# Optimization experiments

Hardware: AMD Instinct MI355X
Metric: run time of the kernel (lower is better)

Reference implementation:

```python
import jax, jax.numpy as jnp
import numpy as np

D_MODEL = 1024
HEADS = 16
HEAD_DIM = D_MODEL // HEADS


def setup_inputs() -> dict:
    key = jax.random.key(0)
    k_x, k_q, k_k, k_v, k_o = jax.random.split(key, 5)
    B, S = 4, 2048
    return {
        "x": jax.random.normal(k_x, (B, S, D_MODEL), dtype=jnp.float32),
        "W_q": jax.random.normal(k_q, (D_MODEL, D_MODEL), dtype=jnp.float32),
        "W_k": jax.random.normal(k_k, (D_MODEL, D_MODEL), dtype=jnp.float32),
        "W_v": jax.random.normal(k_v, (D_MODEL, D_MODEL), dtype=jnp.float32),
        "fc_out": jax.random.normal(k_o, (D_MODEL, D_MODEL), dtype=jnp.float32),
    }


def reference(x, W_q, W_k, W_v, fc_out):
    B, S, D = x.shape
    H, Hd = HEADS, HEAD_DIM
    # QKV projections (no bias)
    Q = jnp.matmul(x, W_q)  # [B,S,D]
    K = jnp.matmul(x, W_k)
    V = jnp.matmul(x, W_v)
    # split heads -> [B,H,S,Hd]
    Qh = Q.reshape(B, S, H, Hd).transpose(0, 2, 1, 3)
    Kh = K.reshape(B, S, H, Hd).transpose(0, 2, 1, 3)
    Vh = V.reshape(B, S, H, Hd).transpose(0, 2, 1, 3)
    # full unfused attention: materialize [B,H,S,S] scores, softmax over last dim
    scores = jnp.einsum("bhqd,bhkd->bhqk", Qh, Kh) / jnp.sqrt(jnp.float32(Hd))
    attn = jax.nn.softmax(scores, axis=-1)
    head_out = jnp.einsum("bhqk,bhkd->bhqd", attn, Vh)  # [B,H,S,Hd]
    merged = head_out.transpose(0, 2, 1, 3).reshape(B, S, D)
    return jnp.matmul(merged, fc_out)
```

## Files before the change

### kernel.cpp

```cpp
#include <hip/hip_runtime.h>
#include <stdint.h>

#define MROWS 8192
#define DM    1024
#define NH    16
#define HD    64
#define SEQ   2048

typedef __bf16 bf16x8 __attribute__((ext_vector_type(8)));
typedef __bf16 bf16x4 __attribute__((ext_vector_type(4)));
typedef float  floatx4 __attribute__((ext_vector_type(4)));

#define QSCALE 0.18033688011112042f

__device__ __forceinline__ int xcd_swz512(int bid) {
  return ((bid & 7) << 6) | (bid >> 3);
}

__device__ __forceinline__ void async16(const void* g, void* l) {
  __builtin_amdgcn_global_load_lds(
      (__attribute__((address_space(1))) void*)g,
      (__attribute__((address_space(3))) void*)l,
      16, 0, 0);
}

__device__ __forceinline__ floatx4 mfma16(bf16x8 a, bf16x8 b, floatx4 c) {
  return __builtin_amdgcn_mfma_f32_16x16x32_bf16(a, b, c, 0, 0, 0);
}


__global__ void __launch_bounds__(256) split_x_kernel(const float* __restrict__ x,
                                                      __bf16* __restrict__ xh,
                                                      __bf16* __restrict__ xl) {
  const int i = blockIdx.x * 256 + threadIdx.x;
  const float4 v = reinterpret_cast<const float4*>(x)[i];
  const float vv[4] = {v.x, v.y, v.z, v.w};
  bf16x4 H, L;
#pragma unroll
  for (int j = 0; j < 4; ++j) {
    const __bf16 h = (__bf16)vv[j];
    H[j] = h;
    L[j] = (__bf16)(vv[j] - (float)h);
  }
  reinterpret_cast<bf16x4*>(xh)[i] = H;
  reinterpret_cast<bf16x4*>(xl)[i] = L;
}

__global__ void __launch_bounds__(256) wtrans4_kernel(
    const float* __restrict__ Wq, const float* __restrict__ Wk,
    const float* __restrict__ Wv, const float* __restrict__ Wf,
    __bf16* __restrict__ Tqh, __bf16* __restrict__ Tql,
    __bf16* __restrict__ Tkh, __bf16* __restrict__ Tkl,
    __bf16* __restrict__ Tvh, __bf16* __restrict__ Tfh) {
  const int which = blockIdx.x >> 10;
  const int blk = blockIdx.x & 1023;
  const float* W = (which == 0) ? Wq : (which == 1) ? Wk : (which == 2) ? Wv : Wf;
  __bf16* Th = (which == 0) ? Tqh : (which == 1) ? Tkh : (which == 2) ? Tvh : Tfh;
  __bf16* Tl = (which == 0) ? Tql : (which == 1) ? Tkl : (__bf16*)nullptr;

  __shared__ float t[32][33];
  const int tx = threadIdx.x & 31, ty = threadIdx.x >> 5;
  const int bx = blk & 31, by = blk >> 5;
#pragma unroll
  for (int j = 0; j < 4; ++j) {
    const int k = by * 32 + ty + j * 8;
    t[ty + j * 8][tx] = W[(size_t)k * DM + bx * 32 + tx];
  }
  __syncthreads();
#pragma unroll
  for (int j = 0; j < 4; ++j) {
    const int n = bx * 32 + ty + j * 8;
    const int k = by * 32 + tx;
    const float v = t[tx][ty + j * 8];
    const __bf16 h = (__bf16)v;
    Th[(size_t)n * DM + k] = h;
    if (Tl) Tl[(size_t)n * DM + k] = (__bf16)(v - (float)h);
  }
}

template <int OUTMODE>
__global__ void __launch_bounds__(256) gemm_nt(const __bf16* __restrict__ Ah,
                                               const __bf16* __restrict__ Bh,
                                               void* __restrict__ C0) {
  __shared__ __align__(16) __bf16 sAh[128 * 32];
  __shared__ __align__(16) __bf16 sBh[128 * 32];

  const int tid = threadIdx.x;
  const int lid = xcd_swz512(blockIdx.x);
  const int bm = lid >> 3;
  const int bn = lid & 7;
  const int m0 = bm << 7, n0 = bn << 7;
  const int w = tid >> 6;
  const int lane = tid & 63;
  const int wm = (w >> 1) << 6;
  const int wn = (w & 1) << 6;
  const int lm = lane & 15;
  const int q4 = lane >> 4;

  floatx4 acc[4][4];
  const floatx4 fz = {0.f, 0.f, 0.f, 0.f};
#pragma unroll
  for (int i = 0; i < 4; ++i)
#pragma unroll
    for (int j = 0; j < 4; ++j) acc[i][j] = fz;

  const int c0 = tid, c1 = tid + 256;
  const int row0 = c0 >> 2, cc0 = (c0 & 3) ^ ((row0 >> 1) & 3);
  const int row1 = c1 >> 2, cc1 = (c1 & 3) ^ ((row1 >> 1) & 3);

  int offA[4], offB[4];
#pragma unroll
  for (int i = 0; i < 4; ++i) {
    const int ra = wm + i * 16 + lm;
    offA[i] = ra * 32 + ((q4 ^ ((ra >> 1) & 3)) << 3);
    const int rb = wn + i * 16 + lm;
    offB[i] = rb * 32 + ((q4 ^ ((rb >> 1) & 3)) << 3);
  }

  size_t ga0 = (size_t)(m0 + row0) * DM + cc0 * 8;
  size_t gb0 = (size_t)(n0 + row0) * DM + cc0 * 8;
  size_t ga1 = (size_t)(m0 + row1) * DM + cc1 * 8;
  size_t gb1 = (size_t)(n0 + row1) * DM + cc1 * 8;

  for (int it = 0; it < 32; ++it) {
    async16(Ah + ga0, &sAh[c0 * 8]);
    async16(Bh + gb0, &sBh[c0 * 8]);
    async16(Ah + ga1, &sAh[c1 * 8]);
    async16(Bh + gb1, &sBh[c1 * 8]);
    ga0 += 32; gb0 += 32; ga1 += 32; gb1 += 32;
    __syncthreads();

    bf16x8 ah[4], bh[4];
#pragma unroll
    for (int i = 0; i < 4; ++i) {
      ah[i] = *(const bf16x8*)&sAh[offA[i]];
      bh[i] = *(const bf16x8*)&sBh[offB[i]];
    }
#pragma unroll
    for (int i = 0; i < 4; ++i)
#pragma unroll
      for (int j = 0; j < 4; ++j)
        acc[i][j] = mfma16(ah[i], bh[j], acc[i][j]);
    __syncthreads();
  }

#pragma unroll
  for (int i = 0; i < 4; ++i) {
#pragma unroll
    for (int j = 0; j < 4; ++j) {
#pragma unroll
      for (int r = 0; r < 4; ++r) {
        const int gr = m0 + wm + i * 16 + q4 * 4 + r;
        const int gc = n0 + wn + j * 16 + lm;
        const float v = acc[i][j][r];
        if constexpr (OUTMODE == 1) {
          ((float*)C0)[(size_t)gr * DM + gc] = v;
        } else {
          const int bb = gr >> 11, ss = gr & 2047;
          const int s6 = ss & 63;
          const int sp = (ss & ~63) | (s6 & 32) | ((s6 & 12) << 1) |
                         ((s6 & 16) >> 2) | (s6 & 3);
          const int hh = gc >> 6, dd = gc & 63;
          ((__bf16*)C0)[(((size_t)(bb * NH + hh) << 6) + dd) * SEQ + sp] = (__bf16)v;
        }
      }
    }
  }
}

__global__ void __launch_bounds__(256, 2) gemm_qk(const __bf16* __restrict__ Ah,
                                                  const __bf16* __restrict__ Al,
                                                  const __bf16* __restrict__ Bqh,
                                                  const __bf16* __restrict__ Bql,
                                                  const __bf16* __restrict__ Bkh,
                                                  const __bf16* __restrict__ Bkl,
                                                  __bf16* __restrict__ Qh,
                                                  __bf16* __restrict__ Ql,
                                                  __bf16* __restrict__ Kh,
                                                  __bf16* __restrict__ Kl) {
  __shared__ __align__(16) __bf16 sAh[128 * 32];
  __shared__ __align__(16) __bf16 sAl[128 * 32];
  __shared__ __align__(16) __bf16 sQh_[128 * 32];
  __shared__ __align__(16) __bf16 sQl_[128 * 32];
  __shared__ __align__(16) __bf16 sKh_[128 * 32];
  __shared__ __align__(16) __bf16 sKl_[128 * 32];

  const int tid = threadIdx.x;
  const int lid = xcd_swz512(blockIdx.x);
  const int bm = lid >> 3;
  const int bn = lid & 7;
  const int m0 = bm << 7, n0 = bn << 7;
  const int w = tid >> 6;
  const int lane = tid & 63;
  const int wm = (w >> 1) << 6;
  const int wn = (w & 1) << 6;
  const int lm = lane & 15;
  const int q4 = lane >> 4;

  floatx4 accq[4][4], acck[4][4];
  const floatx4 fz = {0.f, 0.f, 0.f, 0.f};
#pragma unroll
  for (int i = 0; i < 4; ++i)
#pragma unroll
    for (int j = 0; j < 4; ++j) { accq[i][j] = fz; acck[i][j] = fz; }

  const int c0 = tid, c1 = tid + 256;
  const int row0 = c0 >> 2, cc0 = (c0 & 3) ^ ((row0 >> 1) & 3);
  const int row1 = c1 >> 2, cc1 = (c1 & 3) ^ ((row1 >> 1) & 3);

  int offA[4], offB[4];
#pragma unroll
  for (int i = 0; i < 4; ++i) {
    const int ra = wm + i * 16 + lm;
    offA[i] = ra * 32 + ((q4 ^ ((ra >> 1) & 3)) << 3);
    const int rb = wn + i * 16 + lm;
    offB[i] = rb * 32 + ((q4 ^ ((rb >> 1) & 3)) << 3);
  }

  size_t ga0 = (size_t)(m0 + row0) * DM + cc0 * 8;
  size_t gb0 = (size_t)(n0 + row0) * DM + cc0 * 8;
  size_t ga1 = (size_t)(m0 + row1) * DM + cc1 * 8;
  size_t gb1 = (size_t)(n0 + row1) * DM + cc1 * 8;

  for (int it = 0; it < 32; ++it) {
    async16(Ah + ga0, &sAh[c0 * 8]);
    async16(Al + ga0, &sAl[c0 * 8]);
    async16(Ah + ga1, &sAh[c1 * 8]);
    async16(Al + ga1, &sAl[c1 * 8]);
    async16(Bqh + gb0, &sQh_[c0 * 8]);
    async16(Bql + gb0, &sQl_[c0 * 8]);
    async16(Bqh + gb1, &sQh_[c1 * 8]);
    async16(Bql + gb1, &sQl_[c1 * 8]);
    async16(Bkh + gb0, &sKh_[c0 * 8]);
    async16(Bkl + gb0, &sKl_[c0 * 8]);
    async16(Bkh + gb1, &sKh_[c1 * 8]);
    async16(Bkl + gb1, &sKl_[c1 * 8]);
    ga0 += 32; gb0 += 32; ga1 += 32; gb1 += 32;
    __syncthreads();

    bf16x8 ah[4], al[4];
#pragma unroll
    for (int i = 0; i < 4; ++i) {
      ah[i] = *(const bf16x8*)&sAh[offA[i]];
      al[i] = *(const bf16x8*)&sAl[offA[i]];
    }
    {
      bf16x8 bh[4], bl[4];
#pragma unroll
      for (int j = 0; j < 4; ++j) {
        bh[j] = *(const bf16x8*)&sQh_[offB[j]];
        bl[j] = *(const bf16x8*)&sQl_[offB[j]];
      }
#pragma unroll
      for (int i = 0; i < 4; ++i)
#pragma unroll
        for (int j = 0; j < 4; ++j) {
          accq[i][j] = mfma16(ah[i], bh[j], accq[i][j]);
          accq[i][j] = mfma16(ah[i], bl[j], accq[i][j]);
          accq[i][j] = mfma16(al[i], bh[j], accq[i][j]);
        }
    }
    {
      bf16x8 bh[4], bl[4];
#pragma unroll
      for (int j = 0; j < 4; ++j) {
        bh[j] = *(const bf16x8*)&sKh_[offB[j]];
        bl[j] = *(const bf16x8*)&sKl_[offB[j]];
      }
#pragma unroll
      for (int i = 0; i < 4; ++i)
#pragma unroll
        for (int j = 0; j < 4; ++j) {
          acck[i][j] = mfma16(ah[i], bh[j], acck[i][j]);
          acck[i][j] = mfma16(ah[i], bl[j], acck[i][j]);
          acck[i][j] = mfma16(al[i], bh[j], acck[i][j]);
        }
    }
    __syncthreads();
  }

#pragma unroll
  for (int i = 0; i < 4; ++i) {
#pragma unroll
    for (int j = 0; j < 4; ++j) {
#pragma unroll
      for (int r = 0; r < 4; ++r) {
        const int gr = m0 + wm + i * 16 + q4 * 4 + r;
        const int gc = n0 + wn + j * 16 + lm;
        const size_t idx = (size_t)gr * DM + gc;
        const float vq = accq[i][j][r] * QSCALE;
        const __bf16 qhv = (__bf16)vq;
        Qh[idx] = qhv;
        Ql[idx] = (__bf16)(vq - (float)qhv);
        const float vk = acck[i][j][r];
        const __bf16 khv = (__bf16)vk;
        Kh[idx] = khv;
        Kl[idx] = (__bf16)(vk - (float)khv);
      }
    }
  }
}

__global__ void __launch_bounds__(256, 2) flash_kernel(const __bf16* __restrict__ Qh,
                                                       const __bf16* __restrict__ Ql,
                                                       const __bf16* __restrict__ Kh,
                                                       const __bf16* __restrict__ Kl,
                                                       const __bf16* __restrict__ Vt,
                                                       __bf16* __restrict__ Mg) {
  __shared__ __align__(16) __bf16 sKh[2][64 * 64];
  __shared__ __align__(16) __bf16 sKl[2][64 * 64];
  __shared__ __align__(16) __bf16 sV[2][64 * 64];

  const int tid = threadIdx.x;
  const int lid = xcd_swz512(blockIdx.x);
  const int qt = lid & 7;
  const int bh = lid >> 3;
  const int b = bh >> 4;
  const int h = bh & 15;
  const int mq0 = b * SEQ + qt * 256;
  const int ch = h * 64;
  const int w = tid >> 6;
  const int lane = tid & 63;
  const int lm = lane & 15;
  const int q4 = lane >> 4;

  const int c0 = tid, c1 = tid + 256;
  const int r0 = c0 >> 3, e0 = ((c0 & 7) ^ (r0 & 7)) << 3;
  const int r1 = c1 >> 3, e1 = ((c1 & 7) ^ (r1 & 7)) << 3;

  bf16x8 qh[4][2], ql[4][2];
#pragma unroll
  for (int p = 0; p < 4; ++p) {
    const size_t gq0 = (size_t)(mq0 + p * 64 + r0) * DM + ch + e0;
    const size_t gq1 = (size_t)(mq0 + p * 64 + r1) * DM + ch + e1;
    async16(Qh + gq0, &sKh[0][c0 * 8]);
    async16(Ql + gq0, &sKl[0][c0 * 8]);
    async16(Qh + gq1, &sKh[0][c1 * 8]);
    async16(Ql + gq1, &sKl[0][c1 * 8]);
    __syncthreads();
    if (w == p) {
#pragma unroll
      for (int mi = 0; mi < 4; ++mi) {
        const int rq = mi * 16 + lm;
#pragma unroll
        for (int ks = 0; ks < 2; ++ks) {
          const int oq = rq * 64 + (((ks * 4 + q4) ^ (rq & 7)) << 3);
          qh[mi][ks] = *(const bf16x8*)&sKh[0][oq];
          ql[mi][ks] = *(const bf16x8*)&sKl[0][oq];
        }
      }
    }
    __syncthreads();
  }

  int ofr[2][4];
#pragma unroll
  for (int ks = 0; ks < 2; ++ks)
#pragma unroll
    for (int t = 0; t < 4; ++t) {
      const int rk = t * 16 + lm;
      ofr[ks][t] = rk * 64 + (((ks * 4 + q4) ^ (rk & 7)) << 3);
    }

  floatx4 o[4][4];
  const floatx4 fz = {0.f, 0.f, 0.f, 0.f};
#pragma unroll
  for (int mi = 0; mi < 4; ++mi)
#pragma unroll
    for (int dt = 0; dt < 4; ++dt) o[mi][dt] = fz;
  float lsum[4] = {0.f, 0.f, 0.f, 0.f};
  float m[4] = {-1e30f, -1e30f, -1e30f, -1e30f};

  size_t gk0 = (size_t)(b * SEQ + r0) * DM + ch + e0;
  size_t gk1 = (size_t)(b * SEQ + r1) * DM + ch + e1;
  size_t gv0 = (size_t)(bh * 64 + r0) * SEQ + e0;
  size_t gv1 = (size_t)(bh * 64 + r1) * SEQ + e1;

  async16(Kh + gk0, &sKh[0][c0 * 8]);
  async16(Kl + gk0, &sKl[0][c0 * 8]);
  async16(Kh + gk1, &sKh[0][c1 * 8]);
  async16(Kl + gk1, &sKl[0][c1 * 8]);
  async16(Vt + gv0, &sV[0][c0 * 8]);
  async16(Vt + gv1, &sV[0][c1 * 8]);
  gk0 += (size_t)64 * DM;
  gk1 += (size_t)64 * DM;
  gv0 += 64;
  gv1 += 64;

  for (int it = 0; it < 32; ++it) {
    const int cur = it & 1;
    asm volatile("s_waitcnt vmcnt(0)" ::: "memory");
    __builtin_amdgcn_s_barrier();
    __builtin_amdgcn_sched_barrier(0);
    if (it < 31) {
      const int nxt = cur ^ 1;
      async16(Kh + gk0, &sKh[nxt][c0 * 8]);
      async16(Kl + gk0, &sKl[nxt][c0 * 8]);
      async16(Kh + gk1, &sKh[nxt][c1 * 8]);
      async16(Kl + gk1, &sKl[nxt][c1 * 8]);
      async16(Vt + gv0, &sV[nxt][c0 * 8]);
      async16(Vt + gv1, &sV[nxt][c1 * 8]);
      gk0 += (size_t)64 * DM;
      gk1 += (size_t)64 * DM;
      gv0 += 64;
      gv1 += 64;
    }
    const __bf16* bKh = sKh[cur];
    const __bf16* bKl = sKl[cur];
    const __bf16* bV = sV[cur];

    floatx4 s2[4][4];
#pragma unroll
    for (int nt = 0; nt < 4; ++nt)
#pragma unroll
      for (int mi = 0; mi < 4; ++mi) s2[nt][mi] = fz;
#pragma unroll
    for (int ks = 0; ks < 2; ++ks) {
#pragma unroll
      for (int nt = 0; nt < 4; ++nt) {
        const bf16x8 kh = *(const bf16x8*)&bKh[ofr[ks][nt]];
        const bf16x8 kl = *(const bf16x8*)&bKl[ofr[ks][nt]];
#pragma unroll
        for (int mi = 0; mi < 4; ++mi) {
          s2[nt][mi] = mfma16(kh, qh[mi][ks], s2[nt][mi]);
          s2[nt][mi] = mfma16(kl, qh[mi][ks], s2[nt][mi]);
          s2[nt][mi] = mfma16(kh, ql[mi][ks], s2[nt][mi]);
        }
      }
    }

    float tm[4];
    bool need = false;
#pragma unroll
    for (int mi = 0; mi < 4; ++mi) {
      float mx = fmaxf(fmaxf(s2[0][mi][0], s2[0][mi][1]),
                       fmaxf(s2[0][mi][2], s2[0][mi][3]));
#pragma unroll
      for (int nt = 1; nt < 4; ++nt) {
        mx = fmaxf(mx, fmaxf(fmaxf(s2[nt][mi][0], s2[nt][mi][1]),
                             fmaxf(s2[nt][mi][2], s2[nt][mi][3])));
      }
      mx = fmaxf(mx, __shfl_xor(mx, 16));
      mx = fmaxf(mx, __shfl_xor(mx, 32));
      tm[mi] = mx;
      need = need || (mx > m[mi] + 8.f);
    }
    if (__ballot(need)) {
#pragma unroll
      for (int mi = 0; mi < 4; ++mi) {
        const float mn = fmaxf(m[mi], tm[mi]);
        const float a = __builtin_amdgcn_exp2f(m[mi] - mn);
        m[mi] = mn;
        lsum[mi] *= a;
#pragma unroll
        for (int dt = 0; dt < 4; ++dt) o[mi][dt] *= a;
      }
    }

    bf16x8 aP[4][2];
#pragma unroll
    for (int mi = 0; mi < 4; ++mi) {
      float ps = 0.f;
#pragma unroll
      for (int nt = 0; nt < 4; ++nt) {
#pragma unroll
        for (int r = 0; r < 4; ++r) {
          const float p = __builtin_amdgcn_exp2f(s2[nt][mi][r] - m[mi]);
          ps += p;
          aP[mi][nt >> 1][(nt & 1) * 4 + r] = (__bf16)p;
        }
      }
      ps += __shfl_xor(ps, 16);
      ps += __shfl_xor(ps, 32);
      lsum[mi] += ps;
    }

#pragma unroll
    for (int ks = 0; ks < 2; ++ks) {
#pragma unroll
      for (int dt = 0; dt < 4; ++dt) {
        const bf16x8 bv = *(const bf16x8*)&bV[ofr[ks][dt]];
#pragma unroll
        for (int mi = 0; mi < 4; ++mi)
          o[mi][dt] = mfma16(bv, aP[mi][ks], o[mi][dt]);
      }
    }
  }

#pragma unroll
  for (int mi = 0; mi < 4; ++mi) {
    const float inv = __builtin_amdgcn_rcpf(lsum[mi]);
    const int gr = mq0 + w * 64 + mi * 16 + lm;
#pragma unroll
    for (int dt = 0; dt < 4; ++dt) {
      bf16x4 ov;
#pragma unroll
      for (int r = 0; r < 4; ++r) ov[r] = (__bf16)(o[mi][dt][r] * inv);
      *(bf16x4*)&Mg[(size_t)gr * DM + ch + dt * 16 + q4 * 4] = ov;
    }
  }
}


extern "C" void kernel_launch(void* const* d_in, const int* in_sizes, int n_in,
                              void* d_out, int out_size, void* d_ws, size_t ws_size,
                              hipStream_t stream) {
  (void)in_sizes; (void)n_in; (void)out_size; (void)ws_size;
  const float* x  = (const float*)d_in[0];
  const float* Wq = (const float*)d_in[1];
  const float* Wk = (const float*)d_in[2];
  const float* Wv = (const float*)d_in[3];
  const float* fc = (const float*)d_in[4];
  float* out = (float*)d_out;

  char* base = (char*)d_ws;
  const size_t XB = (size_t)MROWS * DM * 2;
  const size_t WB = (size_t)DM * DM * 2;
  __bf16* xh  = (__bf16*)(base);
  __bf16* xl  = (__bf16*)(base + XB);
  __bf16* wqh = (__bf16*)(base + 2 * XB);
  __bf16* wql = (__bf16*)(base + 2 * XB + WB);
  __bf16* wkh = (__bf16*)(base + 2 * XB + 2 * WB);
  __bf16* wkl = (__bf16*)(base + 2 * XB + 3 * WB);
  __bf16* wvh = (__bf16*)(base + 2 * XB + 4 * WB);
  __bf16* fch = (__bf16*)(base + 2 * XB + 5 * WB);
  __bf16* Qh  = (__bf16*)(base + 2 * XB + 6 * WB);
  __bf16* Ql  = (__bf16*)(base + 3 * XB + 6 * WB);
  __bf16* Kh  = (__bf16*)(base + 4 * XB + 6 * WB);
  __bf16* Kl  = (__bf16*)(base + 5 * XB + 6 * WB);
  __bf16* Vt  = xl;
  __bf16* Mg  = xh;

  split_x_kernel<<<dim3(8192), dim3(256), 0, stream>>>(x, xh, xl);
  wtrans4_kernel<<<dim3(4096), dim3(256), 0, stream>>>(Wq, Wk, Wv, fc,
                                                       wqh, wql, wkh, wkl, wvh, fch);

  gemm_qk<<<dim3(512), dim3(256), 0, stream>>>(xh, xl, wqh, wql, wkh, wkl, Qh, Ql, Kh, Kl);
  gemm_nt<3><<<dim3(512), dim3(256), 0, stream>>>(xh, wvh, (void*)Vt);

  flash_kernel<<<dim3(512), dim3(256), 0, stream>>>(Qh, Ql, Kh, Kl, Vt, Mg);

  gemm_nt<1><<<dim3(512), dim3(256), 0, stream>>>(Mg, fch, (void*)out);
}
```

Before: 374.4 us.

## Double-buffer LDS tiles in gemm_nt to overlap async loads with MFMA

The projection GEMM now keeps two LDS buffers for its A and B tiles. It prefetches the next K-slice with global_load_lds while MFMAs run on the current slice, and uses one wait+barrier per iteration instead of two syncthreads. This is meant to hide global-memory latency that previously stalled each iteration. It doubles the LDS footprint to 32KB per block, which may lower occupancy. The single barrier placement depends on all ds_reads of the buffer being overwritten having finished before the next prefetch is issued.

Measured after the change: 389.3 us. +4.0%, slower.

```diff
diff --git a/kernel.cpp b/kernel.cpp
--- a/kernel.cpp
+++ b/kernel.cpp
@@ -82,8 +82,8 @@
 __global__ void __launch_bounds__(256) gemm_nt(const __bf16* __restrict__ Ah,
                                                const __bf16* __restrict__ Bh,
                                                void* __restrict__ C0) {
-  __shared__ __align__(16) __bf16 sAh[128 * 32];
-  __shared__ __align__(16) __bf16 sBh[128 * 32];
+  __shared__ __align__(16) __bf16 sAh[2][128 * 32];
+  __shared__ __align__(16) __bf16 sBh[2][128 * 32];
 
   const int tid = threadIdx.x;
   const int lid = xcd_swz512(blockIdx.x);
@@ -122,26 +122,37 @@
   size_t ga1 = (size_t)(m0 + row1) * DM + cc1 * 8;
   size_t gb1 = (size_t)(n0 + row1) * DM + cc1 * 8;
 
+  async16(Ah + ga0, &sAh[0][c0 * 8]);
+  async16(Bh + gb0, &sBh[0][c0 * 8]);
+  async16(Ah + ga1, &sAh[0][c1 * 8]);
+  async16(Bh + gb1, &sBh[0][c1 * 8]);
+  ga0 += 32; gb0 += 32; ga1 += 32; gb1 += 32;
+
   for (int it = 0; it < 32; ++it) {
-    async16(Ah + ga0, &sAh[c0 * 8]);
-    async16(Bh + gb0, &sBh[c0 * 8]);
-    async16(Ah + ga1, &sAh[c1 * 8]);
-    async16(Bh + gb1, &sBh[c1 * 8]);
-    ga0 += 32; gb0 += 32; ga1 += 32; gb1 += 32;
-    __syncthreads();
+    const int cur = it & 1;
+    asm volatile("s_waitcnt vmcnt(0)" ::: "memory");
+    __builtin_amdgcn_s_barrier();
+    __builtin_amdgcn_sched_barrier(0);
+    if (it < 31) {
+      const int nxt = cur ^ 1;
+      async16(Ah + ga0, &sAh[nxt][c0 * 8]);
+      async16(Bh + gb0, &sBh[nxt][c0 * 8]);
+      async16(Ah + ga1, &sAh[nxt][c1 * 8]);
+      async16(Bh + gb1, &sBh[nxt][c1 * 8]);
+      ga0 += 32; gb0 += 32; ga1 += 32; gb1 += 32;
+    }
 
     bf16x8 ah[4], bh[4];
 #pragma unroll
     for (int i = 0; i < 4; ++i) {
-      ah[i] = *(const bf16x8*)&sAh[offA[i]];
-      bh[i] = *(const bf16x8*)&sBh[offB[i]];
+      ah[i] = *(const bf16x8*)&sAh[cur][offA[i]];
+      bh[i] = *(const bf16x8*)&sBh[cur][offB[i]];
     }
 #pragma unroll
     for (int i = 0; i < 4; ++i)
 #pragma unroll
       for (int j = 0; j < 4; ++j)
         acc[i][j] = mfma16(ah[i], bh[j], acc[i][j]);
-    __syncthreads();
   }
 
 #pragma unroll
```
